# Kernel tuning notes

Measured on AMD Instinct MI355X. Metric: run time of the kernel, lower is better.

Reference implementation:

```python
import jax, jax.numpy as jnp
import numpy as np

B, T, I, H = 64, 188, 512, 1024
R = H  # recurrent_size == hidden_size (required for the cell math to be consistent)


def setup_inputs() -> dict:
    key = jax.random.key(0)
    ks = jax.random.split(key, 6)
    stdv = 1.0 / np.sqrt(H)
    u = lambda k, shape: jax.random.uniform(k, shape, jnp.float32, -stdv, stdv)
    return {
        "x": jax.random.normal(ks[0], (B, T, I), jnp.float32),
        "h0": jnp.zeros((B, R), jnp.float32),
        "c0": jnp.zeros((B, H), jnp.float32),
        "weight_ih": u(ks[1], (4 * H, I)),
        "weight_hh": u(ks[2], (4 * H, R)),
        "weight_rec": u(ks[3], (2 * R, H)),
        "bias": u(ks[4], (4 * H,)),
        "lengths": jax.random.randint(ks[5], (B,), 1, T + 1),
    }


def reference(x, h0, c0, weight_ih, weight_hh, weight_rec, bias, lengths):
    # length_matrix[j][t] == 1 iff t < lengths[j]; state is zeroed where 0
    mask = (jnp.arange(T)[:, None] < lengths[None, :]).astype(x.dtype)[:, :, None]  # [T,B,1]
    # precompute input projections for all timesteps: [T, B, 4H]
    pre_x = jnp.einsum('bti,gi->tbg', x, weight_ih) + bias

    def step(carry, inp):
        h, c = carry
        px, m = inp
        pre = px + h @ weight_hh.T           # [B, 4H]
        pre_c = c @ weight_rec.T             # [B, 2R] (peephole)
        i = jax.nn.sigmoid(pre[:, :H] + pre_c[:, :H])
        f = jax.nn.sigmoid(pre[:, H:2 * H] + pre_c[:, H:2 * H])
        g = jnp.tanh(pre[:, 2 * H:3 * H])
        c_new = f * c + i * g
        o = jax.nn.sigmoid(pre[:, 3 * H:] + c_new)
        h_new = o * jnp.tanh(c_new)
        h_new = h_new * m  # zero finished sequences (index_fill_ with 0)
        c_new = c_new * m
        return (h_new, c_new), (h_new, c_new)

    (_, _), (hs, cs) = jax.lax.scan(step, (h0, c0), (pre_x, mask))
    # stack over time then transpose(0,1) as in torch -> [B, T, H]
    return jnp.swapaxes(hs, 0, 1), jnp.swapaxes(cs, 0, 1)
```

## Files before the change

### kernel.cpp

```cpp
#include <hip/hip_runtime.h>


#define T_N 188

#define WS_PX     0UL
#define WS_XB     98566144UL
#define WS_WIHB   110886912UL
#define WS_WCOMB  115081216UL
#define WS_HST    127664128UL
#define WS_CST    127926272UL
#define WS_FLAGS  128188416UL
#define WS_WRECLO 128192512UL
#define WS_CSTLO  132386816UL

typedef __attribute__((ext_vector_type(8))) short short8;
typedef __attribute__((ext_vector_type(4))) float f4;
typedef __attribute__((ext_vector_type(4))) int int4v;

__device__ __forceinline__ float b2f(unsigned short u) {
    union { unsigned int i; float f; } v; v.i = ((unsigned int)u) << 16; return v.f;
}
__device__ __forceinline__ unsigned short f2b(float f) {
    unsigned int u = __float_as_uint(f);
    return (unsigned short)((u + 0x7FFFu + ((u >> 16) & 1u)) >> 16);
}
__device__ __forceinline__ float sigf(float x) { return 1.0f / (1.0f + __expf(-x)); }
__device__ __forceinline__ float tanh_(float x) {
    float e = __expf(2.0f * x); return 1.0f - 2.0f / (e + 1.0f);
}
#define MFMA(a, b, c) __builtin_amdgcn_mfma_f32_16x16x32_bf16((a), (b), (c), 0, 0, 0)

#define LD16(dst, addr) \
    asm volatile("global_load_dwordx4 %0, %1, off sc0 sc1" : "=&v"(dst) : "v"(addr))

#define BAL64()                                                            \
    _Pragma("unroll")                                                      \
    for (int u_ = 0; u_ < 16; ++u_) {                                      \
        bl0 = __builtin_fmaf(bl0, 1.0000001f, 1e-7f);                      \
        bl1 = __builtin_fmaf(bl1, 1.0000001f, 2e-7f);                      \
        bl2 = __builtin_fmaf(bl2, 1.0000001f, 3e-7f);                      \
        bl3 = __builtin_fmaf(bl3, 1.0000001f, 4e-7f);                      \
    }

__device__ __forceinline__ f4 px_init(const unsigned short* px, int t, int gate, int jg, int brow) {
    unsigned long long pv =
        *(const unsigned long long*)(px + ((long)(t * 4 + gate) * 1024 + jg) * 64 + brow);
    f4 r;
    r[0] = b2f((unsigned short)pv);
    r[1] = b2f((unsigned short)(pv >> 16));
    r[2] = b2f((unsigned short)(pv >> 32));
    r[3] = b2f((unsigned short)(pv >> 48));
    return r;
}

__global__ void k_prep(const float* __restrict__ x, const float* __restrict__ h0,
                       const float* __restrict__ c0, const float* __restrict__ wih,
                       const float* __restrict__ whh, const float* __restrict__ wrec,
                       unsigned short* __restrict__ xb, unsigned short* __restrict__ wihb,
                       unsigned short* __restrict__ wcomb, unsigned short* __restrict__ hst,
                       unsigned short* __restrict__ cst, unsigned short* __restrict__ wreclo,
                       unsigned short* __restrict__ cstlo, int* __restrict__ flags) {
    const long NX4 = 1540096, NWIH4 = 524288, NWHH4 = 1048576, NWREC4 = 524288, NH4 = 16384;
    const long total = NX4 + NWIH4 + NWHH4 + NWREC4 + NH4 + NH4;
    long gtid = (long)blockIdx.x * blockDim.x + threadIdx.x;
    for (long i = gtid; i < total; i += (long)gridDim.x * blockDim.x) {
        const float* src; unsigned short* dst; unsigned short* lo_dst = nullptr; long off = i;
        if (off < NX4)                   { src = x;    dst = xb; }
        else if ((off -= NX4) < NWIH4)   { src = wih;  dst = wihb; }
        else if ((off -= NWIH4) < NWHH4) { src = whh;  dst = wcomb; }
        else if ((off -= NWHH4) < NWREC4){ src = wrec; dst = wcomb + 4194304; lo_dst = wreclo; }
        else if ((off -= NWREC4) < NH4)  { src = h0;   dst = hst + 65536; }
        else { off -= NH4;                 src = c0;   dst = cst + 65536; lo_dst = cstlo + 65536; }
        float4 v = ((const float4*)src)[off];
        unsigned short hx = f2b(v.x), hy = f2b(v.y), hz = f2b(v.z), hw = f2b(v.w);
        unsigned long long o = (unsigned long long)hx
            | ((unsigned long long)hy << 16)
            | ((unsigned long long)hz << 32)
            | ((unsigned long long)hw << 48);
        *(unsigned long long*)(dst + off * 4) = o;
        if (lo_dst) {
            unsigned long long l = (unsigned long long)f2b(v.x - b2f(hx))
                | ((unsigned long long)f2b(v.y - b2f(hy)) << 16)
                | ((unsigned long long)f2b(v.z - b2f(hz)) << 32)
                | ((unsigned long long)f2b(v.w - b2f(hw)) << 48);
            *(unsigned long long*)(lo_dst + off * 4) = l;
        }
    }
    if (gtid < 1024) flags[gtid] = 0;
}

__global__ void __launch_bounds__(256) k_px(const unsigned short* __restrict__ xb,
                                            const unsigned short* __restrict__ wihb,
                                            const float* __restrict__ bias,
                                            unsigned short* __restrict__ px) {
    const int t = blockIdx.y;
    const int wv = threadIdx.x >> 6, lane = threadIdx.x & 63;
    const int col = lane & 15, quad = lane >> 4;
    const int n = blockIdx.x * 64 + wv * 16 + col;
    const float bn = bias[n];
    f4 acc[4];
#pragma unroll
    for (int mt = 0; mt < 4; ++mt) { acc[mt][0] = bn; acc[mt][1] = bn; acc[mt][2] = bn; acc[mt][3] = bn; }
    const unsigned short* bp = wihb + n * 512 + quad * 8;
#pragma unroll 4
    for (int kk = 0; kk < 16; ++kk) {
        short8 bf = *(const short8*)(bp + kk * 32);
#pragma unroll
        for (int mt = 0; mt < 4; ++mt) {
            const unsigned short* ap = xb + ((mt * 16 + col) * 188 + t) * 512 + kk * 32 + quad * 8;
            short8 af = *(const short8*)ap;
            acc[mt] = MFMA(af, bf, acc[mt]);
        }
    }
    const long pb = ((long)(t * 4 + (n >> 10)) * 1024 + (n & 1023)) * 64;
#pragma unroll
    for (int mt = 0; mt < 4; ++mt) {
        unsigned long long o = (unsigned long long)f2b(acc[mt][0])
            | ((unsigned long long)f2b(acc[mt][1]) << 16)
            | ((unsigned long long)f2b(acc[mt][2]) << 32)
            | ((unsigned long long)f2b(acc[mt][3]) << 48);
        *(unsigned long long*)(px + pb + mt * 16 + quad * 4) = o;
    }
}

__global__ void __launch_bounds__(256, 1) k_scan(
    const unsigned short* __restrict__ wcomb, const unsigned short* __restrict__ wreclo,
    const float* __restrict__ c0, const int* __restrict__ lengths,
    const unsigned short* __restrict__ px, unsigned short* __restrict__ hst,
    unsigned short* __restrict__ cst, unsigned short* __restrict__ cstlo,
    int* __restrict__ flags, float* __restrict__ out) {
    const int cu = blockIdx.x;
    const int g = cu >> 6, cig = cu & 63;
    const int jbase = cig * 16, b0 = g * 16;
    const int tid = threadIdx.x, wv = tid >> 6, lane = tid & 63;
    const int kbase = wv * 256;
    const int col = lane & 15, quad = lane >> 4;
    const int b_ = tid >> 4, j_ = tid & 15;

    __shared__ float pre[2][4][6][16][16];
    __shared__ float c_loc[16][16];
    __shared__ int go_word;

    short8 wg[4][8];
    short8 wh[2][8];
    short8 wl[2][8];
#pragma unroll
    for (int gate = 0; gate < 4; ++gate) {
        const unsigned short* src = wcomb + (long)(gate * 1024 + jbase + col) * 1024 + kbase + quad * 8;
#pragma unroll
        for (int kk = 0; kk < 8; ++kk) wg[gate][kk] = *(const short8*)(src + kk * 32);
    }
#pragma unroll
    for (int tl = 0; tl < 2; ++tl) {
        const unsigned short* sh = wcomb + (long)((4 + tl) * 1024 + jbase + col) * 1024 + kbase + quad * 8;
        const unsigned short* sl = wreclo + (long)(tl * 1024 + jbase + col) * 1024 + kbase + quad * 8;
#pragma unroll
        for (int kk = 0; kk < 8; ++kk) {
            wh[tl][kk] = *(const short8*)(sh + kk * 32);
            wl[tl][kk] = *(const short8*)(sl + kk * 32);
        }
    }
    c_loc[b_][j_] = c0[(b0 + b_) * 1024 + jbase + j_];
    if (tid == 0) go_word = 0;
    const int my_len = lengths[b0 + b_];
    float bl0 = (float)lane + 1.0f, bl1 = bl0 + 0.5f, bl2 = bl0 + 0.25f, bl3 = bl0 + 0.125f;
    __syncthreads();

    float* out_h = out;
    float* out_c = out + 12320768;

    for (int t = 0; t < T_N; ++t) {
        const int sl_r = (t + 1) & 1, sl_w = t & 1, ps = t & 1;

        f4 pxv[4];
        if (wv == 0) {
#pragma unroll
            for (int tile = 0; tile < 4; ++tile)
                pxv[tile] = px_init(px, t, tile, jbase + col, b0 + quad * 4);
        }

        if (t > 0) {
            if (wv == 0) {
                const int* fp = flags + (g * 64 + lane) * 4;
                for (;;) {
                    int4v fvv;
                    asm volatile("global_load_dwordx4 %0, %1, off sc0 sc1" : "=&v"(fvv) : "v"(fp));
                    asm volatile("s_waitcnt vmcnt(0)" ::: "memory");
                    int m0 = fvv[0] < fvv[1] ? fvv[0] : fvv[1];
                    int m1 = fvv[2] < fvv[3] ? fvv[2] : fvv[3];
                    int m = m0 < m1 ? m0 : m1;
                    if (__all(m >= t)) break;
                    BAL64();
                }
                if (lane == 0)
                    __hip_atomic_store(&go_word, t, __ATOMIC_RELAXED, __HIP_MEMORY_SCOPE_WORKGROUP);
            } else {
                for (;;) {
                    int gw = __hip_atomic_load(&go_word, __ATOMIC_RELAXED, __HIP_MEMORY_SCOPE_WORKGROUP);
                    if (gw >= t) break;
                    BAL64();
                }
            }
            asm volatile("" ::: "memory");
        }

        const int sbase = sl_r * 65536 + (b0 + col) * 1024 + kbase + quad * 8;

        short8 hb[8], cb[8], lb[8];
#pragma unroll
        for (int kk = 0; kk < 8; ++kk) LD16(hb[kk], hst + sbase + kk * 32);
#pragma unroll
        for (int kk = 0; kk < 8; ++kk) LD16(cb[kk], cst + sbase + kk * 32);
#pragma unroll
        for (int kk = 0; kk < 8; ++kk) LD16(lb[kk], cstlo + sbase + kk * 32);

        f4 ag0, ag1, ag2, ag3;
        if (wv == 0) { ag0 = pxv[0]; ag1 = pxv[1]; ag2 = pxv[2]; ag3 = pxv[3]; }
        else {
            ag0[0] = 0.f; ag0[1] = 0.f; ag0[2] = 0.f; ag0[3] = 0.f;
            ag1 = ag0; ag2 = ag0; ag3 = ag0;
        }
        f4 ap0 = {0.f, 0.f, 0.f, 0.f}, ap1 = ap0, ap2 = ap0, ap3 = ap0, ap4 = ap0, ap5 = ap0;

        asm volatile("s_waitcnt vmcnt(0)" ::: "memory");
        __builtin_amdgcn_sched_barrier(0);
#pragma unroll
        for (int kk = 0; kk < 8; ++kk) {
            ag0 = MFMA(hb[kk], wg[0][kk], ag0);
            ag1 = MFMA(hb[kk], wg[1][kk], ag1);
            ag2 = MFMA(hb[kk], wg[2][kk], ag2);
            ag3 = MFMA(hb[kk], wg[3][kk], ag3);
            ap0 = MFMA(cb[kk], wh[0][kk], ap0);
            ap1 = MFMA(cb[kk], wh[1][kk], ap1);
            ap2 = MFMA(cb[kk], wl[0][kk], ap2);
            ap3 = MFMA(cb[kk], wl[1][kk], ap3);
            ap4 = MFMA(lb[kk], wh[0][kk], ap4);
            ap5 = MFMA(lb[kk], wh[1][kk], ap5);
        }
#pragma unroll
        for (int r = 0; r < 4; ++r) {
            pre[ps][wv][0][quad * 4 + r][col] = ag0[r];
            pre[ps][wv][1][quad * 4 + r][col] = ag1[r];
            pre[ps][wv][2][quad * 4 + r][col] = ag2[r];
            pre[ps][wv][3][quad * 4 + r][col] = ag3[r];
            pre[ps][wv][4][quad * 4 + r][col] = ap0[r] + ap2[r] + ap4[r];
            pre[ps][wv][5][quad * 4 + r][col] = ap1[r] + ap3[r] + ap5[r];
        }
        __syncthreads();

        float hn, cn;
        {
            float pi = 0.f, pf = 0.f, pg = 0.f, po = 0.f;
#pragma unroll
            for (int q = 0; q < 4; ++q) {
                pi += pre[ps][q][0][b_][j_] + pre[ps][q][4][b_][j_];
                pf += pre[ps][q][1][b_][j_] + pre[ps][q][5][b_][j_];
                pg += pre[ps][q][2][b_][j_];
                po += pre[ps][q][3][b_][j_];
            }
            const float cprev = c_loc[b_][j_];
            const float iv = sigf(pi), fv = sigf(pf), gv = tanh_(pg);
            cn = fv * cprev + iv * gv;
            float ov = sigf(po + cn);
            hn = ov * tanh_(cn);
            if (t >= my_len) { hn = 0.f; cn = 0.f; }
            c_loc[b_][j_] = cn;
            const int sidx = sl_w * 65536 + (b0 + b_) * 1024 + jbase + j_;
            unsigned short hbw  = f2b(hn);
            unsigned short chw  = f2b(cn);
            unsigned short clw  = f2b(cn - b2f(chw));
            __hip_atomic_store(&hst[sidx],   hbw, __ATOMIC_RELAXED, __HIP_MEMORY_SCOPE_AGENT);
            __hip_atomic_store(&cst[sidx],   chw, __ATOMIC_RELAXED, __HIP_MEMORY_SCOPE_AGENT);
            __hip_atomic_store(&cstlo[sidx], clw, __ATOMIC_RELAXED, __HIP_MEMORY_SCOPE_AGENT);
        }
        asm volatile("s_waitcnt vmcnt(0)" ::: "memory");
        if (lane == 0)
            __hip_atomic_store(&flags[cu * 4 + wv], t + 1,
                               __ATOMIC_RELAXED, __HIP_MEMORY_SCOPE_AGENT);
        const long ob = (long)(b0 + b_) * 192512 + (long)t * 1024 + jbase + j_;
        out_h[ob] = hn;
        out_c[ob] = cn;
    }
    asm volatile("" :: "v"(bl0), "v"(bl1), "v"(bl2), "v"(bl3));
}

extern "C" void kernel_launch(void* const* d_in, const int* in_sizes, int n_in,
                              void* d_out, int out_size, void* d_ws, size_t ws_size,
                              hipStream_t stream) {
    const float* x    = (const float*)d_in[0];
    const float* h0   = (const float*)d_in[1];
    const float* c0   = (const float*)d_in[2];
    const float* wih  = (const float*)d_in[3];
    const float* whh  = (const float*)d_in[4];
    const float* wrec = (const float*)d_in[5];
    const float* bias = (const float*)d_in[6];
    const int* lengths = (const int*)d_in[7];

    char* ws = (char*)d_ws;
    unsigned short* px     = (unsigned short*)(ws + WS_PX);
    unsigned short* xb     = (unsigned short*)(ws + WS_XB);
    unsigned short* wihb   = (unsigned short*)(ws + WS_WIHB);
    unsigned short* wcomb  = (unsigned short*)(ws + WS_WCOMB);
    unsigned short* hst    = (unsigned short*)(ws + WS_HST);
    unsigned short* cst    = (unsigned short*)(ws + WS_CST);
    unsigned short* wreclo = (unsigned short*)(ws + WS_WRECLO);
    unsigned short* cstlo  = (unsigned short*)(ws + WS_CSTLO);
    int* flags             = (int*)(ws + WS_FLAGS);
    float* out = (float*)d_out;

    hipLaunchKernelGGL(k_prep, dim3(2048), dim3(256), 0, stream,
                       x, h0, c0, wih, whh, wrec, xb, wihb, wcomb, hst, cst, wreclo, cstlo, flags);
    hipLaunchKernelGGL(k_px, dim3(64, 188), dim3(256), 0, stream, xb, wihb, bias, px);
    hipLaunchKernelGGL(k_scan, dim3(256), dim3(256), 0, stream,
                       wcomb, wreclo, c0, lengths, px, hst, cst, cstlo, flags, out);
}
```

Baseline: 1.691 ms.

## Replace flag-based grid barrier with LSB-tagged state polling and staged vector stores

Drops the per-wave flag array and workgroup go-word handshake. Consumers now poll the state buffers directly, using a generation tag encoded in the low mantissa bit of every bf16 word, so data arrival itself acts as the synchronization signal and one round-trip is saved. The epilogue stages h/c hi/lo values in LDS and writes them with 16-byte vector stores. It also adds an h low-part (hstlo) with extra MFMAs for higher precision, and moves the wrec low-part weights from registers to LDS. Stealing the mantissa LSB costs precision, and polling four full buffers raises load traffic per spin.

```diff
diff --git a/kernel.cpp b/kernel.cpp
--- a/kernel.cpp
+++ b/kernel.cpp
@@ -12,10 +12,10 @@
 #define WS_FLAGS  128188416UL
 #define WS_WRECLO 128192512UL
 #define WS_CSTLO  132386816UL
+#define WS_HSTLO  132648960UL
 
 typedef __attribute__((ext_vector_type(8))) short short8;
 typedef __attribute__((ext_vector_type(4))) float f4;
-typedef __attribute__((ext_vector_type(4))) int int4v;
 
 __device__ __forceinline__ float b2f(unsigned short u) {
     union { unsigned int i; float f; } v; v.i = ((unsigned int)u) << 16; return v.f;
@@ -32,6 +32,13 @@
 
 #define LD16(dst, addr) \
     asm volatile("global_load_dwordx4 %0, %1, off sc0 sc1" : "=&v"(dst) : "v"(addr))
+#define ST16(addr, data) \
+    asm volatile("global_store_dwordx4 %0, %1, off sc0 sc1" :: "v"(addr), "v"(data) : "memory")
+
+__device__ __forceinline__ unsigned int tagxor(short8 v, unsigned int pat) {
+    union { short8 s; unsigned int d[4]; } u; u.s = v;
+    return (u.d[0] ^ pat) | (u.d[1] ^ pat) | (u.d[2] ^ pat) | (u.d[3] ^ pat);
+}
 
 #define BAL64()                                                            \
     _Pragma("unroll")                                                      \
@@ -59,31 +66,39 @@
                        unsigned short* __restrict__ xb, unsigned short* __restrict__ wihb,
                        unsigned short* __restrict__ wcomb, unsigned short* __restrict__ hst,
                        unsigned short* __restrict__ cst, unsigned short* __restrict__ wreclo,
-                       unsigned short* __restrict__ cstlo, int* __restrict__ flags) {
+                       unsigned short* __restrict__ cstlo, unsigned short* __restrict__ hstlo,
+                       int* __restrict__ flags) {
     const long NX4 = 1540096, NWIH4 = 524288, NWHH4 = 1048576, NWREC4 = 524288, NH4 = 16384;
     const long total = NX4 + NWIH4 + NWHH4 + NWREC4 + NH4 + NH4;
     long gtid = (long)blockIdx.x * blockDim.x + threadIdx.x;
     for (long i = gtid; i < total; i += (long)gridDim.x * blockDim.x) {
         const float* src; unsigned short* dst; unsigned short* lo_dst = nullptr; long off = i;
+        bool tag_state = false;
         if (off < NX4)                   { src = x;    dst = xb; }
         else if ((off -= NX4) < NWIH4)   { src = wih;  dst = wihb; }
         else if ((off -= NWIH4) < NWHH4) { src = whh;  dst = wcomb; }
         else if ((off -= NWHH4) < NWREC4){ src = wrec; dst = wcomb + 4194304; lo_dst = wreclo; }
-        else if ((off -= NWREC4) < NH4)  { src = h0;   dst = hst + 65536; }
-        else { off -= NH4;                 src = c0;   dst = cst + 65536; lo_dst = cstlo + 65536; }
+        else if ((off -= NWREC4) < NH4)  { src = h0;   dst = hst; lo_dst = hstlo; tag_state = true; }
+        else { off -= NH4;  src = c0;  dst = cst; lo_dst = cstlo; tag_state = true; }
         float4 v = ((const float4*)src)[off];
         unsigned short hx = f2b(v.x), hy = f2b(v.y), hz = f2b(v.z), hw = f2b(v.w);
+        if (tag_state) { hx |= 1u; hy |= 1u; hz |= 1u; hw |= 1u; }
         unsigned long long o = (unsigned long long)hx
             | ((unsigned long long)hy << 16)
             | ((unsigned long long)hz << 32)
             | ((unsigned long long)hw << 48);
         *(unsigned long long*)(dst + off * 4) = o;
+        if (tag_state) *(unsigned long long*)(dst + 65536 + off * 4) = o;
         if (lo_dst) {
-            unsigned long long l = (unsigned long long)f2b(v.x - b2f(hx))
-                | ((unsigned long long)f2b(v.y - b2f(hy)) << 16)
-                | ((unsigned long long)f2b(v.z - b2f(hz)) << 32)
-                | ((unsigned long long)f2b(v.w - b2f(hw)) << 48);
+            unsigned short lx = f2b(v.x - b2f(hx)), ly = f2b(v.y - b2f(hy));
+            unsigned short lz = f2b(v.z - b2f(hz)), lw = f2b(v.w - b2f(hw));
+            if (tag_state) { lx |= 1u; ly |= 1u; lz |= 1u; lw |= 1u; }
+            unsigned long long l = (unsigned long long)lx
+                | ((unsigned long long)ly << 16)
+                | ((unsigned long long)lz << 32)
+                | ((unsigned long long)lw << 48);
             *(unsigned long long*)(lo_dst + off * 4) = l;
+            if (tag_state) *(unsigned long long*)(lo_dst + 65536 + off * 4) = l;
         }
     }
     if (gtid < 1024) flags[gtid] = 0;
@@ -128,7 +143,8 @@
     const float* __restrict__ c0, const int* __restrict__ lengths,
     const unsigned short* __restrict__ px, unsigned short* __restrict__ hst,
     unsigned short* __restrict__ cst, unsigned short* __restrict__ cstlo,
-    int* __restrict__ flags, float* __restrict__ out) {
+    unsigned short* __restrict__ hstlo, int* __restrict__ flags,
+    float* __restrict__ out) {
     const int cu = blockIdx.x;
     const int g = cu >> 6, cig = cu & 63;
     const int jbase = cig * 16, b0 = g * 16;
@@ -139,11 +155,11 @@
 
     __shared__ float pre[2][4][6][16][16];
     __shared__ float c_loc[16][16];
-    __shared__ int go_word;
+    __shared__ __align__(16) unsigned short epi[4][16][16];
+    __shared__ __align__(16) unsigned short wlds[4][2][8][512];
 
     short8 wg[4][8];
     short8 wh[2][8];
-    short8 wl[2][8];
 #pragma unroll
     for (int gate = 0; gate < 4; ++gate) {
         const unsigned short* src = wcomb + (long)(gate * 1024 + jbase + col) * 1024 + kbase + quad * 8;
@@ -157,11 +173,10 @@
 #pragma unroll
         for (int kk = 0; kk < 8; ++kk) {
             wh[tl][kk] = *(const short8*)(sh + kk * 32);
-            wl[tl][kk] = *(const short8*)(sl + kk * 32);
+            *(short8*)&wlds[wv][tl][kk][lane * 8] = *(const short8*)(sl + kk * 32);
         }
     }
     c_loc[b_][j_] = c0[(b0 + b_) * 1024 + jbase + j_];
-    if (tid == 0) go_word = 0;
     const int my_len = lengths[b0 + b_];
     float bl0 = (float)lane + 1.0f, bl1 = bl0 + 0.5f, bl2 = bl0 + 0.25f, bl3 = bl0 + 0.125f;
     __syncthreads();
@@ -171,6 +186,11 @@
 
     for (int t = 0; t < T_N; ++t) {
         const int sl_r = (t + 1) & 1, sl_w = t & 1, ps = t & 1;
+        const int genr = (t == 0) ? 3 : (((t - 1) >> 1) & 3);
+        const unsigned int pat = (unsigned int)(genr & 1)
+                               | ((unsigned int)((genr >> 1) & 1) << 16);
+        const int gw = (t >> 1) & 3;
+        const unsigned int tb = (unsigned int)((j_ & 1) ? ((gw >> 1) & 1) : (gw & 1));
 
         f4 pxv[4];
         if (wv == 0) {
@@ -179,40 +199,31 @@
                 pxv[tile] = px_init(px, t, tile, jbase + col, b0 + quad * 4);
         }
 
-        if (t > 0) {
-            if (wv == 0) {
-                const int* fp = flags + (g * 64 + lane) * 4;
-                for (;;) {
-                    int4v fvv;
-                    asm volatile("global_load_dwordx4 %0, %1, off sc0 sc1" : "=&v"(fvv) : "v"(fp));
-                    asm volatile("s_waitcnt vmcnt(0)" ::: "memory");
-                    int m0 = fvv[0] < fvv[1] ? fvv[0] : fvv[1];
-                    int m1 = fvv[2] < fvv[3] ? fvv[2] : fvv[3];
-                    int m = m0 < m1 ? m0 : m1;
-                    if (__all(m >= t)) break;
-                    BAL64();
-                }
-                if (lane == 0)
-                    __hip_atomic_store(&go_word, t, __ATOMIC_RELAXED, __HIP_MEMORY_SCOPE_WORKGROUP);
-            } else {
-                for (;;) {
-                    int gw = __hip_atomic_load(&go_word, __ATOMIC_RELAXED, __HIP_MEMORY_SCOPE_WORKGROUP);
-                    if (gw >= t) break;
-                    BAL64();
-                }
+        const int sbase = sl_r * 65536 + (b0 + col) * 1024 + kbase + quad * 8;
+
+        short8 hb[8], hlb[8], cb[8], lb[8];
+        for (;;) {
+#pragma unroll
+            for (int kk = 0; kk < 8; ++kk) LD16(hb[kk], hst + sbase + kk * 32);
+#pragma unroll
+            for (int kk = 0; kk < 8; ++kk) LD16(hlb[kk], hstlo + sbase + kk * 32);
+#pragma unroll
+            for (int kk = 0; kk < 8; ++kk) LD16(cb[kk], cst + sbase + kk * 32);
+#pragma unroll
+            for (int kk = 0; kk < 8; ++kk) LD16(lb[kk], cstlo + sbase + kk * 32);
+            asm volatile("s_waitcnt vmcnt(0)" ::: "memory");
+            __builtin_amdgcn_sched_barrier(0);
+            unsigned int bad = 0;
+#pragma unroll
+            for (int kk = 0; kk < 8; ++kk) {
+                bad |= tagxor(hb[kk], pat);
+                bad |= tagxor(hlb[kk], pat);
+                bad |= tagxor(cb[kk], pat);
+                bad |= tagxor(lb[kk], pat);
             }
-            asm volatile("" ::: "memory");
-        }
-
-        const int sbase = sl_r * 65536 + (b0 + col) * 1024 + kbase + quad * 8;
-
-        short8 hb[8], cb[8], lb[8];
-#pragma unroll
-        for (int kk = 0; kk < 8; ++kk) LD16(hb[kk], hst + sbase + kk * 32);
-#pragma unroll
-        for (int kk = 0; kk < 8; ++kk) LD16(cb[kk], cst + sbase + kk * 32);
-#pragma unroll
-        for (int kk = 0; kk < 8; ++kk) LD16(lb[kk], cstlo + sbase + kk * 32);
+            if (__all((bad & 0x00010001u) == 0u)) break;
+            BAL64();
+        }
 
         f4 ag0, ag1, ag2, ag3;
         if (wv == 0) { ag0 = pxv[0]; ag1 = pxv[1]; ag2 = pxv[2]; ag3 = pxv[3]; }
@@ -222,20 +233,27 @@
         }
         f4 ap0 = {0.f, 0.f, 0.f, 0.f}, ap1 = ap0, ap2 = ap0, ap3 = ap0, ap4 = ap0, ap5 = ap0;
 
-        asm volatile("s_waitcnt vmcnt(0)" ::: "memory");
-        __builtin_amdgcn_sched_barrier(0);
 #pragma unroll
         for (int kk = 0; kk < 8; ++kk) {
+            short8 lw0 = *(const short8*)&wlds[wv][0][kk][lane * 8];
+            short8 lw1 = *(const short8*)&wlds[wv][1][kk][lane * 8];
             ag0 = MFMA(hb[kk], wg[0][kk], ag0);
             ag1 = MFMA(hb[kk], wg[1][kk], ag1);
             ag2 = MFMA(hb[kk], wg[2][kk], ag2);
             ag3 = MFMA(hb[kk], wg[3][kk], ag3);
             ap0 = MFMA(cb[kk], wh[0][kk], ap0);
             ap1 = MFMA(cb[kk], wh[1][kk], ap1);
-            ap2 = MFMA(cb[kk], wl[0][kk], ap2);
-            ap3 = MFMA(cb[kk], wl[1][kk], ap3);
+            ap2 = MFMA(cb[kk], lw0, ap2);
+            ap3 = MFMA(cb[kk], lw1, ap3);
             ap4 = MFMA(lb[kk], wh[0][kk], ap4);
             ap5 = MFMA(lb[kk], wh[1][kk], ap5);
+        }
+#pragma unroll
+        for (int kk = 0; kk < 8; ++kk) {
+            ag0 = MFMA(hlb[kk], wg[0][kk], ag0);
+            ag1 = MFMA(hlb[kk], wg[1][kk], ag1);
+            ag2 = MFMA(hlb[kk], wg[2][kk], ag2);
+            ag3 = MFMA(hlb[kk], wg[3][kk], ag3);
         }
 #pragma unroll
         for (int r = 0; r < 4; ++r) {
@@ -265,18 +283,24 @@
             hn = ov * tanh_(cn);
             if (t >= my_len) { hn = 0.f; cn = 0.f; }
             c_loc[b_][j_] = cn;
-            const int sidx = sl_w * 65536 + (b0 + b_) * 1024 + jbase + j_;
-            unsigned short hbw  = f2b(hn);
-            unsigned short chw  = f2b(cn);
-            unsigned short clw  = f2b(cn - b2f(chw));
-            __hip_atomic_store(&hst[sidx],   hbw, __ATOMIC_RELAXED, __HIP_MEMORY_SCOPE_AGENT);
-            __hip_atomic_store(&cst[sidx],   chw, __ATOMIC_RELAXED, __HIP_MEMORY_SCOPE_AGENT);
-            __hip_atomic_store(&cstlo[sidx], clw, __ATOMIC_RELAXED, __HIP_MEMORY_SCOPE_AGENT);
-        }
-        asm volatile("s_waitcnt vmcnt(0)" ::: "memory");
-        if (lane == 0)
-            __hip_atomic_store(&flags[cu * 4 + wv], t + 1,
-                               __ATOMIC_RELAXED, __HIP_MEMORY_SCOPE_AGENT);
+            unsigned short hhw = (unsigned short)((f2b(hn) & 0xFFFEu) | tb);
+            unsigned short chw = (unsigned short)((f2b(cn) & 0xFFFEu) | tb);
+            unsigned short hlw = (unsigned short)((f2b(hn - b2f(hhw)) & 0xFFFEu) | tb);
+            unsigned short clw = (unsigned short)((f2b(cn - b2f(chw)) & 0xFFFEu) | tb);
+            epi[0][b_][j_] = hhw;
+            epi[1][b_][j_] = hlw;
+            epi[2][b_][j_] = chw;
+            epi[3][b_][j_] = clw;
+        }
+        __syncthreads();
+
+        if (tid < 128) {
+            const int a = tid >> 5, cidx = tid & 31, row = cidx >> 1, q = cidx & 1;
+            short8 v = *(const short8*)&epi[a][row][q * 8];
+            unsigned short* arr = (a == 0) ? hst : (a == 1) ? hstlo : (a == 2) ? cst : cstlo;
+            unsigned short* dstp = arr + sl_w * 65536 + (b0 + row) * 1024 + jbase + q * 8;
+            ST16(dstp, v);
+        }
         const long ob = (long)(b0 + b_) * 192512 + (long)t * 1024 + jbase + j_;
         out_h[ob] = hn;
         out_c[ob] = cn;
@@ -305,12 +329,14 @@
     unsigned short* cst    = (unsigned short*)(ws + WS_CST);
     unsigned short* wreclo = (unsigned short*)(ws + WS_WRECLO);
     unsigned short* cstlo  = (unsigned short*)(ws + WS_CSTLO);
+    unsigned short* hstlo  = (unsigned short*)(ws + WS_HSTLO);
     int* flags             = (int*)(ws + WS_FLAGS);
     float* out = (float*)d_out;
 
     hipLaunchKernelGGL(k_prep, dim3(2048), dim3(256), 0, stream,
-                       x, h0, c0, wih, whh, wrec, xb, wihb, wcomb, hst, cst, wreclo, cstlo, flags);
+                       x, h0, c0, wih, whh, wrec, xb, wihb, wcomb, hst, cst, wreclo,
+                       cstlo, hstlo, flags);
     hipLaunchKernelGGL(k_px, dim3(64, 188), dim3(256), 0, stream, xb, wihb, bias, px);
     hipLaunchKernelGGL(k_scan, dim3(256), dim3(256), 0, stream,
-                       wcomb, wreclo, c0, lengths, px, hst, cst, cstlo, flags, out);
-}
+                       wcomb, wreclo, c0, lengths, px, hst, cst, cstlo, hstlo, flags, out);
+}
```

New measurement: 2.230 ms. +31.9%, slower.
